# Kernel tuning notes

Hardware: AMD Instinct MI355X
Metric: run time of the kernel (lower is better)

Reference implementation:

```python
import jax, jax.numpy as jnp
import numpy as np

NTOKEN = 32000
NINP = 512
NHIDLAST = 1024
N_EXPERTS = 10
N = 1024


def setup_inputs() -> dict:
    key = jax.random.key(0)
    ks = jax.random.split(key, 4)
    return {
        "output": jax.random.normal(ks[0], (N, NHIDLAST), dtype=jnp.float32),
        "W_latent": jax.random.normal(ks[1], (N_EXPERTS * NINP, NHIDLAST), dtype=jnp.float32) * 0.02,
        "b_latent": jnp.zeros((N_EXPERTS * NINP,), dtype=jnp.float32),
        "W_decoder": jax.random.normal(ks[2], (NTOKEN, NINP), dtype=jnp.float32) * 0.02,
        "b_decoder": jnp.zeros((NTOKEN,), dtype=jnp.float32),
        "W_reduce": jax.random.normal(ks[3], (N_EXPERTS, NHIDLAST), dtype=jnp.float32) * 0.02,
        "b_reduce": jnp.zeros((N_EXPERTS,), dtype=jnp.float32),
        "dropoutl": 0,
    }


def reference(output, W_latent, b_latent, W_decoder, b_decoder, W_reduce, b_reduce, dropoutl):
    n = output.shape[0]
    # latent projection + tanh; lockdrop with rate 0 is identity
    latent = jnp.tanh(output @ W_latent.T + b_latent)            # [N, E*ninp]
    logit = latent.reshape(n * N_EXPERTS, NINP) @ W_decoder.T + b_decoder  # [N*E, V]
    # stick-breaking Beta parameters
    a = jax.nn.softplus(output @ W_reduce.T + b_reduce) + 1e-8   # [N, E]
    b = jnp.sum(a, axis=1)                                       # [N]
    c = jnp.cumsum(a, axis=1)                                    # [N, E]
    d = jnp.abs(b[:, None] - c)                                  # remaining mass
    d = jnp.maximum(d, 1e-8)  # last column is exactly 0; avoid Beta(a,0) NaN
    sample = jax.random.beta(jax.random.key(42), a, d)           # reparameterized Beta
    # rem @ diag(ones, offset=1) shifts columns right by one; rem[:,0]=1
    rem = 1.0 - sample
    rem_shift = jnp.concatenate([jnp.ones((n, 1), dtype=rem.dtype), rem[:, :-1]], axis=1)
    remprod = jnp.cumprod(rem_shift, axis=1)
    pis = remprod * sample                                       # [N, E] mixture weights
    prob = jax.nn.softmax(logit.reshape(n, N_EXPERTS, NTOKEN), axis=-1)
    out = jnp.einsum('net,ne->nt', prob, pis)                    # [N, V]
    return out
```

## Files before the change

kernel.cpp:

```cpp
#include <hip/hip_runtime.h>
#include <cstdint>
#include <cstddef>

#pragma clang fp contract(off)

#define NTOK  32000
#define NINP  512
#define NHID  1024
#define NEXP  10
#define NROW  1024
#define NLAT  (NEXP*NINP)
#define MROWS (NROW*NEXP)

typedef __attribute__((ext_vector_type(4))) float f32x4;
typedef __attribute__((ext_vector_type(8))) short bf16x8;
typedef __attribute__((ext_vector_type(8))) unsigned short us16x8;

#define GLD16(g, l) __builtin_amdgcn_global_load_lds(                       \
    (const __attribute__((address_space(1))) void*)(g),                     \
    (__attribute__((address_space(3))) void*)(l), 16, 0, 0)

__device__ __forceinline__ unsigned short f2b(float x) {
    uint32_t u = __float_as_uint(x);
    uint32_t r = (u + 0x7fffu + ((u >> 16) & 1u)) >> 16;
    return (unsigned short)r;
}
__device__ __forceinline__ float b2f(unsigned short b) {
    return __uint_as_float(((uint32_t)b) << 16);
}

__device__ __forceinline__ uint32_t rotl32(uint32_t v, int r) {
    return (v << r) | (v >> (32 - r));
}

__device__ __forceinline__ void threefry(uint32_t k0, uint32_t k1,
                                         uint32_t x0, uint32_t x1,
                                         uint32_t& o0, uint32_t& o1) {
    uint32_t k2 = k0 ^ k1 ^ 0x1BD11BDAu;
    x0 += k0; x1 += k1;
#define TF_R(r) { x0 += x1; x1 = rotl32(x1, r); x1 ^= x0; }
    TF_R(13) TF_R(15) TF_R(26) TF_R(6)
    x0 += k1; x1 += k2 + 1u;
    TF_R(17) TF_R(29) TF_R(16) TF_R(24)
    x0 += k2; x1 += k0 + 2u;
    TF_R(13) TF_R(15) TF_R(26) TF_R(6)
    x0 += k0; x1 += k1 + 3u;
    TF_R(17) TF_R(29) TF_R(16) TF_R(24)
    x0 += k1; x1 += k2 + 4u;
    TF_R(13) TF_R(15) TF_R(26) TF_R(6)
    x0 += k2; x1 += k0 + 5u;
#undef TF_R
    o0 = x0; o1 = x1;
}

struct RKey { uint32_t a, b; };

__device__ __forceinline__ RKey kfold(RKey k, uint32_t i) {
    RKey r; threefry(k.a, k.b, 0u, i, r.a, r.b); return r;
}
__device__ __forceinline__ uint32_t kbits(RKey k) {
    uint32_t o0, o1; threefry(k.a, k.b, 0u, 0u, o0, o1); return o0 ^ o1;
}
__device__ __forceinline__ float u01(RKey k) {
    uint32_t b = (kbits(k) >> 9) | 0x3f800000u;
    return __uint_as_float(b) - 1.0f;
}
__device__ __forceinline__ float erfinv_xla(float x) {
    float xx = x * x;
    float w = -log1pf(-xx);
    float p;
    if (w < 5.0f) {
        float ww = w - 2.5f;
        p = 2.81022636e-08f;
        p = p * ww; p = p + 3.43273939e-07f;
        p = p * ww; p = p + -3.5233877e-06f;
        p = p * ww; p = p + -4.39150654e-06f;
        p = p * ww; p = p + 0.00021858087f;
        p = p * ww; p = p + -0.00125372503f;
        p = p * ww; p = p + -0.00417768164f;
        p = p * ww; p = p + 0.246640727f;
        p = p * ww; p = p + 1.50140941f;
    } else {
        float ww = sqrtf(w) - 3.0f;
        p = -0.000200214257f;
        p = p * ww; p = p + 0.000100950558f;
        p = p * ww; p = p + 0.00134934322f;
        p = p * ww; p = p + -0.00367342844f;
        p = p * ww; p = p + 0.00573950773f;
        p = p * ww; p = p + -0.0076224613f;
        p = p * ww; p = p + 0.00943887047f;
        p = p * ww; p = p + 1.00167406f;
        p = p * ww; p = p + 2.83297682f;
    }
    return p * x;
}
__device__ __forceinline__ float norm1(RKey k) {
    const float lo = -0.99999994f;
    float f = u01(k);
    float u = f * 2.0f;
    u = u + lo;
    u = fmaxf(lo, u);
    return 1.41421356f * erfinv_xla(u);
}

__device__ float gamma_log(RKey key, float alpha) {
    const float one_third = 0.33333334f;
    bool boost = (alpha >= 1.0f);
    float alpha_orig = alpha;
    if (!boost) alpha = alpha + 1.0f;
    float d = alpha - one_third;
    float c = one_third / sqrtf(d);

    RKey sub = kfold(key, 1u);
    key      = kfold(key, 0u);
    float log_boost = 0.0f;
    if (!boost) {
        float uB = u01(sub);
        log_boost = log1pf(-uB) * (1.0f / alpha_orig);
    }

    float X = 0.f, V = 1.f, U = 2.f;
    int guard = 0;
    do {
        RKey xk = kfold(key, 1u);
        RKey Uk = kfold(key, 2u);
        key     = kfold(key, 0u);
        float x = 0.f, v = -1.f;
        RKey kin = xk;
        int g2 = 0;
        do {
            RKey sk = kfold(kin, 1u);
            kin     = kfold(kin, 0u);
            x = norm1(sk);
            float cx = x * c;
            v = 1.0f + cx;
        } while (v <= 0.0f && ++g2 < 256);
        X = x * x;
        V = (v * v) * v;
        U = u01(Uk);
        float sq = 1.0f - 0.0331f * (X * X);
        if (U < sq) break;
        float bound = (X * 0.5f) + ((d - d * V) + d * logf(V));
        if (logf(U) < bound) break;
    } while (++guard < 256);

    float ls = logf(d) + logf(V);
    ls = ls + log_boost;
    return ls;
}

__global__ void k_a(const float* __restrict__ out_in,
                    const float* __restrict__ Wred,
                    const float* __restrict__ bred,
                    float* __restrict__ a_arr, float* __restrict__ dpar) {
    int n = blockIdx.x;
    int lane = threadIdx.x;
    __shared__ float zred[NEXP];
    const float* orow = out_in + (size_t)n * NHID;
    for (int e = 0; e < NEXP; ++e) {
        const float* wrow = Wred + (size_t)e * NHID;
        float s = 0.f;
        for (int k = lane; k < NHID; k += 64) s += orow[k] * wrow[k];
        for (int off = 32; off; off >>= 1) s += __shfl_xor(s, off);
        if (lane == 0) zred[e] = s + bred[e];
    }
    __syncthreads();
    if (lane == 0) {
        float a[NEXP];
        float b = 0.f;
        for (int e = 0; e < NEXP; ++e) {
            float z = zred[e];
            a[e] = fmaxf(z, 0.f) + log1pf(expf(-fabsf(z))) + 1e-8f;
        }
        for (int e = 0; e < NEXP; ++e) b += a[e];
        float cs = 0.f;
        for (int e = 0; e < NEXP; ++e) {
            cs += a[e];
            float dd = fmaxf(fabsf(b - cs), 1e-8f);
            a_arr[n * NEXP + e] = a[e];
            dpar [n * NEXP + e] = dd;
        }
    }
}

__global__ void k_sample(const float* __restrict__ a_arr,
                         const float* __restrict__ dpar,
                         float* __restrict__ sample) {
    int i = blockIdx.x * 256 + threadIdx.x;
    if (i >= MROWS) return;
    RKey root{0u, 42u};
    RKey ka = kfold(root, 0u);
    RKey kb = kfold(root, 1u);
    float lga = gamma_log(kfold(ka, (uint32_t)i), a_arr[i]);
    float lgb = gamma_log(kfold(kb, (uint32_t)i), dpar[i]);
    float lm = fmaxf(lga, lgb);
    float ea = expf(lga - lm), eb = expf(lgb - lm);
    sample[i] = ea / (ea + eb);
}

__global__ void k_pis(const float* __restrict__ sample, float* __restrict__ pis) {
    int n = blockIdx.x * blockDim.x + threadIdx.x;
    if (n >= NROW) return;
    float rp = 1.0f;
    for (int e = 0; e < NEXP; ++e) {
        float s = sample[n * NEXP + e];
        pis[n * NEXP + e] = rp * s;
        rp = rp * (1.0f - s);
    }
}

__global__ void k_w(const float* __restrict__ pis, const float* __restrict__ Z,
                    float* __restrict__ w, int r0, int cnt) {
    int i = blockIdx.x * 256 + threadIdx.x;
    if (i >= cnt) return;
    int r = r0 + i;
    w[r] = pis[r] / Z[r];
}

__global__ void k_cvt(const float* __restrict__ src, unsigned short* __restrict__ dst, int n) {
    int i = (blockIdx.x * 256 + threadIdx.x) * 8;
    if (i >= n) return;
    float4 v0 = *(const float4*)(src + i);
    float4 v1 = *(const float4*)(src + i + 4);
    us16x8 o;
    o[0] = f2b(v0.x); o[1] = f2b(v0.y); o[2] = f2b(v0.z); o[3] = f2b(v0.w);
    o[4] = f2b(v1.x); o[5] = f2b(v1.y); o[6] = f2b(v1.z); o[7] = f2b(v1.w);
    *(us16x8*)(dst + i) = o;
}

__device__ __forceinline__ void combine_span(const unsigned short* __restrict__ P,
                                             const float* __restrict__ pis,
                                             const float* __restrict__ Z,
                                             float* __restrict__ out,
                                             int n0, int items, int idx0, int stride) {
    for (int idx = idx0; idx < items; idx += stride) {
        int nl = idx / 4000;
        int c8 = (idx - nl * 4000) * 8;
        int n  = n0 + nl;
        float w[NEXP];
#pragma unroll
        for (int e = 0; e < NEXP; ++e)
            w[e] = pis[n * NEXP + e] / Z[n * NEXP + e];
        float s[8] = {0.f,0.f,0.f,0.f,0.f,0.f,0.f,0.f};
        const unsigned short* Pr = P + (size_t)nl * NEXP * NTOK + c8;
#pragma unroll
        for (int e = 0; e < NEXP; ++e) {
            us16x8 v = __builtin_nontemporal_load((const us16x8*)(Pr + (size_t)e * NTOK));
#pragma unroll
            for (int jj = 0; jj < 8; ++jj)
                s[jj] = s[jj] + w[e] * b2f(v[jj]);
        }
        float* orow = out + (size_t)n * NTOK + c8;
        f32x4 o0 = {s[0], s[1], s[2], s[3]};
        f32x4 o1 = {s[4], s[5], s[6], s[7]};
        __builtin_nontemporal_store(o0, (f32x4*)(orow));
        __builtin_nontemporal_store(o1, (f32x4*)(orow + 4));
    }
}

__global__ __launch_bounds__(256)
void k_fin(const unsigned short* __restrict__ P,
           const float* __restrict__ pis,
           const float* __restrict__ Z,
           float* __restrict__ out, int n0, int items) {
    combine_span(P, pis, Z, out, n0, items,
                 (int)(blockIdx.x * 256u + threadIdx.x),
                 (int)(gridDim.x * 256u));
}

__global__ __launch_bounds__(256)
void k_latm(const unsigned short* __restrict__ A,
            const unsigned short* __restrict__ B,
            const float* __restrict__ bias,
            unsigned short* __restrict__ dst) {
    __shared__ unsigned short Als[2][128 * 64];
    __shared__ unsigned short Bls[2][128 * 64];
    const int tid  = threadIdx.x;
    const int lane = tid & 63, wid = tid >> 6;
    const int wm = wid >> 1, wn = wid & 1;
    const uint32_t l = blockIdx.x;
    const int row0 = (int)(l & 7u) * 128;
    const int col0 = (int)(l >> 3) * 128;
    const int lrow8 = lane >> 3, lslot = lane & 7;

    const unsigned short* pA[4];
    const unsigned short* pB[4];
#pragma unroll
    for (int i = 0; i < 4; ++i) {
        int rA = wid * 32 + i * 8 + lrow8;
        pA[i] = A + (size_t)(row0 + rA) * NHID + ((lslot ^ (rA & 7)) << 3);
        int rB = wid * 32 + i * 8 + lrow8;
        pB[i] = B + (size_t)(col0 + rB) * NHID + ((lslot ^ (rB & 7)) << 3);
    }
    int offA[2][4], offB[2][4];
#pragma unroll
    for (int kh = 0; kh < 2; ++kh)
#pragma unroll
        for (int f = 0; f < 4; ++f) {
            int rA = wm * 64 + f * 16 + (lane & 15);
            offA[kh][f] = rA * 128 + ((((lane >> 4) * 16) + kh * 64) ^ ((rA & 7) << 4));
            int rB = wn * 64 + f * 16 + (lane & 15);
            offB[kh][f] = rB * 128 + ((((lane >> 4) * 16) + kh * 64) ^ ((rB & 7) << 4));
        }

    f32x4 acc[4][4];
#pragma unroll
    for (int mf = 0; mf < 4; ++mf)
#pragma unroll
        for (int nf = 0; nf < 4; ++nf) acc[mf][nf] = (f32x4)0.f;

#pragma unroll
    for (int i = 0; i < 4; ++i) {
        GLD16(pA[i], (char*)&Als[0][0] + (wid * 32 + i * 8) * 128); pA[i] += 64;
        GLD16(pB[i], (char*)&Bls[0][0] + (wid * 32 + i * 8) * 128); pB[i] += 64;
    }
    __syncthreads();

#pragma unroll
    for (int t = 0; t < 16; ++t) {
        const int cur = t & 1, nxt = cur ^ 1;
        if (t < 15) {
#pragma unroll
            for (int i = 0; i < 4; ++i) {
                GLD16(pA[i], (char*)&Als[nxt][0] + (wid * 32 + i * 8) * 128); pA[i] += 64;
                GLD16(pB[i], (char*)&Bls[nxt][0] + (wid * 32 + i * 8) * 128); pB[i] += 64;
            }
        }
        const char* Ab = (const char*)&Als[cur][0];
        const char* Bb = (const char*)&Bls[cur][0];
#pragma unroll
        for (int kh = 0; kh < 2; ++kh) {
            bf16x8 af[4], bfr[4];
#pragma unroll
            for (int f = 0; f < 4; ++f) {
                af[f]  = *(const bf16x8*)(Ab + offA[kh][f]);
                bfr[f] = *(const bf16x8*)(Bb + offB[kh][f]);
            }
#pragma unroll
            for (int mf = 0; mf < 4; ++mf)
#pragma unroll
                for (int nf = 0; nf < 4; ++nf)
                    acc[mf][nf] = __builtin_amdgcn_mfma_f32_16x16x32_bf16(
                        af[mf], bfr[nf], acc[mf][nf], 0, 0, 0);
        }
        __syncthreads();
    }

    const int q = lane >> 4, cl = lane & 15;
#pragma unroll
    for (int mf = 0; mf < 4; ++mf) {
#pragma unroll
        for (int nf = 0; nf < 4; ++nf) {
            int col = col0 + wn * 64 + nf * 16 + cl;
            float bc = bias[col];
#pragma unroll
            for (int j = 0; j < 4; ++j) {
                int r = row0 + wm * 64 + mf * 16 + q * 4 + j;
                dst[(size_t)r * NLAT + col] = f2b(tanhf(acc[mf][nf][j] + bc));
            }
        }
    }
}

template<int MODE>
__global__ __launch_bounds__(256)
void k_dec(const unsigned short* __restrict__ A,
           const unsigned short* __restrict__ B,
           const float* __restrict__ bias,
           const float* __restrict__ wmix,
           float* __restrict__ dst,
           unsigned short* __restrict__ Pst,
           int rb0, int nRB, int nGemm,
           const float* __restrict__ pis,
           const float* __restrict__ Zarr,
           float* __restrict__ outp,
           const unsigned short* __restrict__ Pprev,
           int n0prev, int itemsPrev) {
    if (MODE == 3 && (int)blockIdx.x >= nGemm) {
        const int cb = (int)blockIdx.x - nGemm;
        combine_span(Pprev, pis, Zarr, outp, n0prev, itemsPrev,
                     cb * 256 + (int)threadIdx.x,
                     ((int)gridDim.x - nGemm) * 256);
        return;
    }
    __shared__ __align__(16) unsigned char lds_raw[73728];
    unsigned short (*Als)[160 * 64] = (unsigned short (*)[160 * 64])lds_raw;
    unsigned short (*Bls)[128 * 64] = (unsigned short (*)[128 * 64])(lds_raw + 40960);
    const int tid  = threadIdx.x;
    const int lane = tid & 63, wid = tid >> 6;
    const int wm = wid >> 1, wn = wid & 1;
    const uint32_t l = blockIdx.x;
    int by_l, bx;
    if (nRB >= 8 && (nRB & 7) == 0) {
        const int per = nRB >> 3;
        const uint32_t jb = l >> 3;
        by_l = (int)(l & 7u) * per + (int)(jb % (uint32_t)per);
        bx   = (int)(jb / (uint32_t)per);
    } else {
        by_l = (int)(l % (uint32_t)nRB);
        bx   = (int)(l / (uint32_t)nRB);
    }
    const int by   = rb0 + by_l;
    const int row0 = by * 160;
    const int rl0  = by_l * 160;
    const int col0 = bx * 128;
    const int lrow8 = lane >> 3, lslot = lane & 7;

    const unsigned short* pA[5];
    const unsigned short* pB[4];
#pragma unroll
    for (int i = 0; i < 5; ++i) {
        int rA = wid * 40 + i * 8 + lrow8;
        pA[i] = A + (size_t)(row0 + rA) * 512 + ((lslot ^ (rA & 7)) << 3);
    }
#pragma unroll
    for (int i = 0; i < 4; ++i) {
        int rB = wid * 32 + i * 8 + lrow8;
        pB[i] = B + (size_t)(col0 + rB) * 512 + ((lslot ^ (rB & 7)) << 3);
    }
    int offA[2][5], offB[2][4];
#pragma unroll
    for (int kh = 0; kh < 2; ++kh) {
#pragma unroll
        for (int mf = 0; mf < 5; ++mf) {
            int r = wm * 80 + mf * 16 + (lane & 15);
            offA[kh][mf] = r * 128 + ((((lane >> 4) * 16) + kh * 64) ^ ((r & 7) << 4));
        }
#pragma unroll
        for (int nf = 0; nf < 4; ++nf) {
            int r = wn * 64 + nf * 16 + (lane & 15);
            offB[kh][nf] = r * 128 + ((((lane >> 4) * 16) + kh * 64) ^ ((r & 7) << 4));
        }
    }

    f32x4 acc[5][4];
#pragma unroll
    for (int mf = 0; mf < 5; ++mf)
#pragma unroll
        for (int nf = 0; nf < 4; ++nf) acc[mf][nf] = (f32x4)0.f;

#pragma unroll
    for (int i = 0; i < 5; ++i) {
        GLD16(pA[i], (char*)&Als[0][0] + (wid * 40 + i * 8) * 128); pA[i] += 64;
    }
#pragma unroll
    for (int i = 0; i < 4; ++i) {
        GLD16(pB[i], (char*)&Bls[0][0] + (wid * 32 + i * 8) * 128); pB[i] += 64;
    }
    __syncthreads();

#pragma unroll
    for (int t = 0; t < 8; ++t) {
        const int cur = t & 1, nxt = cur ^ 1;
        if (t < 7) {
#pragma unroll
            for (int i = 0; i < 5; ++i) {
                GLD16(pA[i], (char*)&Als[nxt][0] + (wid * 40 + i * 8) * 128); pA[i] += 64;
            }
#pragma unroll
            for (int i = 0; i < 4; ++i) {
                GLD16(pB[i], (char*)&Bls[nxt][0] + (wid * 32 + i * 8) * 128); pB[i] += 64;
            }
        }
        const char* Ab = (const char*)&Als[cur][0];
        const char* Bb = (const char*)&Bls[cur][0];
#pragma unroll
        for (int kh = 0; kh < 2; ++kh) {
            bf16x8 af[5], bfr[4];
#pragma unroll
            for (int mf = 0; mf < 5; ++mf)
                af[mf] = *(const bf16x8*)(Ab + offA[kh][mf]);
#pragma unroll
            for (int nf = 0; nf < 4; ++nf)
                bfr[nf] = *(const bf16x8*)(Bb + offB[kh][nf]);
#pragma unroll
            for (int mf = 0; mf < 5; ++mf)
#pragma unroll
                for (int nf = 0; nf < 4; ++nf)
                    acc[mf][nf] = __builtin_amdgcn_mfma_f32_16x16x32_bf16(
                        af[mf], bfr[nf], acc[mf][nf], 0, 0, 0);
        }
        __syncthreads();
    }

    const int q = lane >> 4, cl = lane & 15;
    float bv[4];
#pragma unroll
    for (int nf = 0; nf < 4; ++nf) bv[nf] = bias[col0 + wn * 64 + nf * 16 + cl];

    if (MODE == 3) {
#pragma unroll
        for (int mf = 0; mf < 5; ++mf) {
#pragma unroll
            for (int jj = 0; jj < 4; ++jj) {
                const int rr = wm * 80 + mf * 16 + q * 4 + jj;
                float p0 = expf(acc[mf][0][jj] + bv[0]);
                float p1 = expf(acc[mf][1][jj] + bv[1]);
                float p2 = expf(acc[mf][2][jj] + bv[2]);
                float p3 = expf(acc[mf][3][jj] + bv[3]);
                float s = ((p0 + p1) + (p2 + p3));
                s += __shfl_xor(s, 1); s += __shfl_xor(s, 2);
                s += __shfl_xor(s, 4); s += __shfl_xor(s, 8);
                if (cl == 0) atomicAdd(&dst[row0 + rr], s);
                unsigned short* lrow = (unsigned short*)(lds_raw + rr * 288);
                lrow[wn * 64 + cl]      = f2b(p0);
                lrow[wn * 64 + 16 + cl] = f2b(p1);
                lrow[wn * 64 + 32 + cl] = f2b(p2);
                lrow[wn * 64 + 48 + cl] = f2b(p3);
            }
        }
        __syncthreads();
        const int rloc = tid >> 4, c16 = tid & 15;
#pragma unroll
        for (int it = 0; it < 10; ++it) {
            int gr = it * 16 + rloc;
            us16x8 v = *(const us16x8*)(lds_raw + gr * 288 + c16 * 16);
            __builtin_nontemporal_store(
                v, (us16x8*)(Pst + (size_t)(rl0 + gr) * NTOK + col0 + c16 * 8));
        }
    } else if (MODE == 1) {
#pragma unroll
        for (int mf = 0; mf < 5; ++mf) {
#pragma unroll
            for (int jj = 0; jj < 4; ++jj) {
                const int rr = wm * 80 + mf * 16 + q * 4 + jj;
                float p0 = expf(acc[mf][0][jj] + bv[0]);
                float p1 = expf(acc[mf][1][jj] + bv[1]);
                float p2 = expf(acc[mf][2][jj] + bv[2]);
                float p3 = expf(acc[mf][3][jj] + bv[3]);
                float s = ((p0 + p1) + (p2 + p3));
                s += __shfl_xor(s, 1); s += __shfl_xor(s, 2);
                s += __shfl_xor(s, 4); s += __shfl_xor(s, 8);
                if (cl == 0) atomicAdd(&dst[row0 + rr], s);
            }
        }
    } else {
        float wv[5][4];
#pragma unroll
        for (int mf = 0; mf < 5; ++mf)
#pragma unroll
            for (int jj = 0; jj < 4; ++jj)
                wv[mf][jj] = wmix[row0 + wm * 80 + mf * 16 + q * 4 + jj];
#pragma unroll
        for (int mf = 0; mf < 5; ++mf)
#pragma unroll
            for (int nf = 0; nf < 4; ++nf)
#pragma unroll
                for (int jj = 0; jj < 4; ++jj)
                    acc[mf][nf][jj] = wv[mf][jj] * expf(acc[mf][nf][jj] + bv[nf]);

        const int tok0 = by * 16 + wm * 8;
#pragma unroll
        for (int t = 0; t < 8; ++t) {
#pragma unroll
            for (int nf = 0; nf < 4; ++nf) {
                float s = 0.f;
#pragma unroll
                for (int i = 0; i < 10; ++i) {
                    const int rl = 10 * t + i;
                    const int mf = rl >> 4, qr = (rl >> 2) & 3, jj = rl & 3;
                    s += (q == qr) ? acc[mf][nf][jj] : 0.f;
                }
                s += __shfl_xor(s, 16);
                s += __shfl_xor(s, 32);
                if (q == 0)
                    dst[(size_t)(tok0 + t) * NTOK + col0 + wn * 64 + nf * 16 + cl] = s;
            }
        }
    }
}

extern "C" void kernel_launch(void* const* d_in, const int* in_sizes, int n_in,
                              void* d_out, int out_size, void* d_ws, size_t ws_size,
                              hipStream_t stream) {
    const float* output    = (const float*)d_in[0];
    const float* W_latent  = (const float*)d_in[1];
    const float* b_latent  = (const float*)d_in[2];
    const float* W_decoder = (const float*)d_in[3];
    const float* b_decoder = (const float*)d_in[4];
    const float* W_reduce  = (const float*)d_in[5];
    const float* b_reduce  = (const float*)d_in[6];
    float* out = (float*)d_out;

    char* wsb = (char*)d_ws;
    unsigned short* latb  = (unsigned short*)wsb;
    unsigned short* wdecb = (unsigned short*)(wsb + 10485760);
    float* a_arr  = (float*)(wsb + 10485760 + 32768000);
    float* dpar   = a_arr  + MROWS;
    float* sample = dpar   + MROWS;
    float* pis    = sample + MROWS;
    float* Z      = pis    + MROWS;
    float* wmix   = Z      + MROWS;
    unsigned short* Pbuf = (unsigned short*)(wmix + MROWS);
    const size_t BASE = 10485760ull + 32768000ull + 6ull * MROWS * 4ull;
    const size_t avail = (ws_size > BASE) ? (ws_size - BASE) : 0;

    int CRd = 0, CRs = 0;
    {
        const int cands[4] = {2560, 1280, 640, 320};
        for (int c = 0; c < 4; ++c)
            if (2ull * (size_t)cands[c] * NTOK * 2ull <= avail) { CRd = cands[c]; break; }
        if (CRd == 0) {
            const int cs[5] = {2560, 1280, 640, 320, 160};
            for (int c = 0; c < 5; ++c)
                if ((size_t)cs[c] * NTOK * 2ull <= avail) { CRs = cs[c]; break; }
        }
    }

    unsigned short* outb  = (unsigned short*)d_out;
    unsigned short* wlatb = (unsigned short*)((char*)d_out + 2097152);

    k_a<<<NROW, 64, 0, stream>>>(output, W_reduce, b_reduce, a_arr, dpar);
    k_sample<<<MROWS / 256, 256, 0, stream>>>(a_arr, dpar, sample);
    k_pis<<<(NROW + 255) / 256, 256, 0, stream>>>(sample, pis);

    k_cvt<<<(NTOK * NINP) / 2048, 256, 0, stream>>>(W_decoder, wdecb, NTOK * NINP);
    k_cvt<<<(NROW * NHID) / 2048, 256, 0, stream>>>(output, outb, NROW * NHID);
    k_cvt<<<(NLAT * NHID) / 2048, 256, 0, stream>>>(W_latent, wlatb, NLAT * NHID);

    k_latm<<<320, 256, 0, stream>>>(outb, wlatb, b_latent, latb);

    (void)hipMemsetAsync(Z, 0, MROWS * sizeof(float), stream);

    if (CRd > 0) {
        const int nRB = CRd / 160, nGemm = nRB * 250, nch = MROWS / CRd;
        const int items = (CRd / 10) * 4000;
        for (int ci = 0; ci < nch; ++ci) {
            unsigned short* Pcur  = Pbuf + (size_t)(ci & 1) * CRd * NTOK;
            unsigned short* Pprev = Pbuf + (size_t)((ci & 1) ^ 1) * CRd * NTOK;
            const int extra = (ci > 0) ? 1000 : 0;
            k_dec<3><<<nGemm + extra, 256, 0, stream>>>(
                latb, wdecb, b_decoder, nullptr, Z, Pcur, ci * nRB, nRB, nGemm,
                pis, Z, out, Pprev, (ci - 1) * (CRd / 10), items);
        }
        unsigned short* Plast = Pbuf + (size_t)((nch - 1) & 1) * CRd * NTOK;
        k_fin<<<items / 256, 256, 0, stream>>>(Plast, pis, Z, out,
                                               (nch - 1) * (CRd / 10), items);
    } else if (CRs > 0) {
        const int nRB = CRs / 160;
        const int items = (CRs / 10) * 4000;
        for (int r0 = 0; r0 < MROWS; r0 += CRs) {
            k_dec<3><<<nRB * 250, 256, 0, stream>>>(
                latb, wdecb, b_decoder, nullptr, Z, Pbuf, r0 / 160, nRB, 1 << 30,
                pis, Z, out, nullptr, 0, 0);
            k_fin<<<items / 256, 256, 0, stream>>>(Pbuf, pis, Z, out, r0 / 10, items);
        }
    } else {
        k_dec<1><<<16000, 256, 0, stream>>>(latb, wdecb, b_decoder, nullptr, Z,
                                            nullptr, 0, 64, 1 << 30,
                                            pis, Z, out, nullptr, 0, 0);
        k_w<<<MROWS / 256, 256, 0, stream>>>(pis, Z, wmix, 0, MROWS);
        k_dec<2><<<16000, 256, 0, stream>>>(latb, wdecb, b_decoder, wmix, out,
                                            nullptr, 0, 64, 1 << 30,
                                            pis, Z, out, nullptr, 0, 0);
    }
    (void)in_sizes; (void)n_in; (void)out_size;
}
```

Baseline: 823.3 us.

## Prefetch two K-stages ahead with explicit vmcnt waits and raw barriers

Restructures the double-buffered K loop so two stages are issued up front. Each refill is issued after the compute barrier and followed by a partial s_waitcnt vmcnt(9), so one stage's global-to-LDS loads stay in flight while the other is consumed. The aim is to hide more memory latency than the old issue-next-then-sync pattern, at the cost of an extra barrier per iteration and hand-managed counters that must match the load count. The LDS row stride for the bf16 probability staging also changes from 288 to 272 bytes, altering the bank-conflict pattern.

```diff
diff --git a/kernel.cpp b/kernel.cpp
--- a/kernel.cpp
+++ b/kernel.cpp
@@ -439,29 +439,27 @@
 #pragma unroll
         for (int nf = 0; nf < 4; ++nf) acc[mf][nf] = (f32x4)0.f;
 
-#pragma unroll
-    for (int i = 0; i < 5; ++i) {
-        GLD16(pA[i], (char*)&Als[0][0] + (wid * 40 + i * 8) * 128); pA[i] += 64;
-    }
-#pragma unroll
-    for (int i = 0; i < 4; ++i) {
-        GLD16(pB[i], (char*)&Bls[0][0] + (wid * 32 + i * 8) * 128); pB[i] += 64;
-    }
-    __syncthreads();
+    auto stage = [&](int b) {
+#pragma unroll
+        for (int i = 0; i < 5; ++i) {
+            GLD16(pA[i], (char*)&Als[b][0] + (wid * 40 + i * 8) * 128); pA[i] += 64;
+        }
+#pragma unroll
+        for (int i = 0; i < 4; ++i) {
+            GLD16(pB[i], (char*)&Bls[b][0] + (wid * 32 + i * 8) * 128); pB[i] += 64;
+        }
+    };
+
+    stage(0);
+    stage(1);
+    asm volatile("s_waitcnt vmcnt(9)" ::: "memory");
+    __builtin_amdgcn_sched_barrier(0);
+    __builtin_amdgcn_s_barrier();
+    __builtin_amdgcn_sched_barrier(0);
 
 #pragma unroll
     for (int t = 0; t < 8; ++t) {
-        const int cur = t & 1, nxt = cur ^ 1;
-        if (t < 7) {
-#pragma unroll
-            for (int i = 0; i < 5; ++i) {
-                GLD16(pA[i], (char*)&Als[nxt][0] + (wid * 40 + i * 8) * 128); pA[i] += 64;
-            }
-#pragma unroll
-            for (int i = 0; i < 4; ++i) {
-                GLD16(pB[i], (char*)&Bls[nxt][0] + (wid * 32 + i * 8) * 128); pB[i] += 64;
-            }
-        }
+        const int cur = t & 1;
         const char* Ab = (const char*)&Als[cur][0];
         const char* Bb = (const char*)&Bls[cur][0];
 #pragma unroll
@@ -480,7 +478,21 @@
                     acc[mf][nf] = __builtin_amdgcn_mfma_f32_16x16x32_bf16(
                         af[mf], bfr[nf], acc[mf][nf], 0, 0, 0);
         }
-        __syncthreads();
+        __builtin_amdgcn_sched_barrier(0);
+        __builtin_amdgcn_s_barrier();
+        __builtin_amdgcn_sched_barrier(0);
+        if (t < 6) {
+            stage(cur);
+            asm volatile("s_waitcnt vmcnt(9)" ::: "memory");
+            __builtin_amdgcn_sched_barrier(0);
+            __builtin_amdgcn_s_barrier();
+            __builtin_amdgcn_sched_barrier(0);
+        } else if (t == 6) {
+            asm volatile("s_waitcnt vmcnt(0)" ::: "memory");
+            __builtin_amdgcn_sched_barrier(0);
+            __builtin_amdgcn_s_barrier();
+            __builtin_amdgcn_sched_barrier(0);
+        }
     }
 
     const int q = lane >> 4, cl = lane & 15;
@@ -502,7 +514,7 @@
                 s += __shfl_xor(s, 1); s += __shfl_xor(s, 2);
                 s += __shfl_xor(s, 4); s += __shfl_xor(s, 8);
                 if (cl == 0) atomicAdd(&dst[row0 + rr], s);
-                unsigned short* lrow = (unsigned short*)(lds_raw + rr * 288);
+                unsigned short* lrow = (unsigned short*)(lds_raw + rr * 272);
                 lrow[wn * 64 + cl]      = f2b(p0);
                 lrow[wn * 64 + 16 + cl] = f2b(p1);
                 lrow[wn * 64 + 32 + cl] = f2b(p2);
@@ -514,7 +526,7 @@
 #pragma unroll
         for (int it = 0; it < 10; ++it) {
             int gr = it * 16 + rloc;
-            us16x8 v = *(const us16x8*)(lds_raw + gr * 288 + c16 * 16);
+            us16x8 v = *(const us16x8*)(lds_raw + gr * 272 + c16 * 16);
             __builtin_nontemporal_store(
                 v, (us16x8*)(Pst + (size_t)(rl0 + gr) * NTOK + col0 + c16 * 8));
         }
```

Result: slower. 1.064 ms (+29.3%).
